# Kernel tuning notes

Hardware: AMD Instinct MI355X
Metric: run time of the kernel (lower is better)

Reference implementation:

```python
import jax, jax.numpy as jnp
import numpy as np

B, S, E, H = 2, 2048, 1024, 16
D = E // H  # head_dim = 64


def setup_inputs() -> dict:
    key = jax.random.key(0)
    ks = jax.random.split(key, 6)
    sc = 1.0 / np.sqrt(D)
    return {
        "x": jax.random.normal(ks[0], (B, S, E), dtype=jnp.float32),
        "Wq": jax.random.normal(ks[1], (D, D), dtype=jnp.float32) * sc,
        "Wk": jax.random.normal(ks[2], (D, D), dtype=jnp.float32) * sc,
        "Wv": jax.random.normal(ks[3], (D, D), dtype=jnp.float32) * sc,
        "Wo": jax.random.normal(ks[4], (E, E), dtype=jnp.float32) * (1.0 / np.sqrt(E)),
        "bo": jnp.zeros((E,), dtype=jnp.float32),
    }


def reference(x, Wq, Wk, Wv, Wo, bo):
    b, s, e = x.shape
    # split into heads: (B, H, S, D)
    xh = x.reshape(b, s, H, D).transpose(0, 2, 1, 3)
    # per-head linear projections (weights SHARED across heads); torch Linear: x @ W^T
    q = jnp.einsum('bhsd,ed->bhse', xh, Wq)
    k = jnp.einsum('bhsd,ed->bhse', xh, Wk)
    v = jnp.einsum('bhsd,ed->bhse', xh, Wv)
    # full attention matrix (B, H, S, S) — faithful to the naive original
    energy = jnp.einsum('bhqd,bhkd->bhqk', q, k)
    attn = jax.nn.softmax(energy / jnp.sqrt(jnp.asarray(D, x.dtype)), axis=-1)
    out = jnp.einsum('bhqk,bhkd->bhqd', attn, v)
    out = out.transpose(0, 2, 1, 3).reshape(b, s, e)
    return out @ Wo.T + bo
```

## Files before the change

### kernel.cpp

```cpp
#include <hip/hip_runtime.h>
#include <hip/hip_bf16.h>

#define B 2
#define S 2048
#define E 1024
#define H 16
#define D 64

typedef unsigned short ushort_t;
typedef __attribute__((ext_vector_type(8))) short bf16x8;
typedef __attribute__((ext_vector_type(4))) float f32x4;
typedef __attribute__((ext_vector_type(16))) float f32x16;

static __device__ __forceinline__ ushort_t f2bf(float f) {
    union { float f; unsigned u; } v; v.f = f;
    unsigned r = v.u + 0x7fffu + ((v.u >> 16) & 1u);
    return (ushort_t)(r >> 16);
}

#define MFMA(a, b, c)   __builtin_amdgcn_mfma_f32_16x16x32_bf16((a), (b), (c), 0, 0, 0)
#define MFMA32(a, b, c) __builtin_amdgcn_mfma_f32_32x32x16_bf16((a), (b), (c), 0, 0, 0)
#define PACKBF(hi, lo) __builtin_amdgcn_perm((hi), (lo), 0x07060302u)

__global__ __launch_bounds__(256) void cvt_w(
    const float* __restrict__ Wq, const float* __restrict__ Wk, const float* __restrict__ Wv,
    const float* __restrict__ Wo,
    ushort_t* __restrict__ wqb, ushort_t* __restrict__ wkb, ushort_t* __restrict__ wvb,
    ushort_t* __restrict__ wob)
{
    int gid = blockIdx.x, t = threadIdx.x;
    if (gid < 1024) {
        int i = gid * 1024 + t * 4;
        float4 f = *(const float4*)(Wo + i);
        ushort4 u; u.x = f2bf(f.x); u.y = f2bf(f.y); u.z = f2bf(f.z); u.w = f2bf(f.w);
        *(ushort4*)(wob + i) = u;
    } else {
        int idx = (gid - 1024) * 1024 + t * 4;
        int which = idx >> 12, off = idx & 4095;
        const float* src = (which == 0) ? Wq : (which == 1) ? Wk : Wv;
        ushort_t* dst    = (which == 0) ? wqb : (which == 1) ? wkb : wvb;
        float sc = (which == 0) ? 0.18033688011112042f : 1.0f;
        float4 f = *(const float4*)(src + off);
        ushort4 u; u.x = f2bf(f.x * sc); u.y = f2bf(f.y * sc);
        u.z = f2bf(f.z * sc); u.w = f2bf(f.w * sc);
        *(ushort4*)(dst + off) = u;
    }
}

__global__ __launch_bounds__(256) void qkv_proj(
    const float* __restrict__ x,
    const ushort_t* __restrict__ wq, const ushort_t* __restrict__ wk, const ushort_t* __restrict__ wv,
    ushort_t* __restrict__ q, ushort_t* __restrict__ k, ushort_t* __restrict__ vT)
{
    __shared__ ushort_t Xs[64][72];
    __shared__ ushort_t Wqs[64][72], Wks[64][72], Wvs[64][72];
    int t = threadIdx.x;
    int bh = blockIdx.y, b = bh >> 4, h = bh & 15;
    int s0 = blockIdx.x * 64;

    {
        int i = t >> 2, d0 = (t & 3) * 16;
        const float* xp = x + ((size_t)(b * S + s0 + i)) * E + h * D + d0;
        #pragma unroll
        for (int c = 0; c < 16; c += 4) {
            float4 f = *(const float4*)(xp + c);
            Xs[i][d0 + c + 0] = f2bf(f.x); Xs[i][d0 + c + 1] = f2bf(f.y);
            Xs[i][d0 + c + 2] = f2bf(f.z); Xs[i][d0 + c + 3] = f2bf(f.w);
        }
    }
    {
        int e = t >> 2, d0 = (t & 3) * 16;
        *(bf16x8*)&Wqs[e][d0]     = *(const bf16x8*)(wq + e * 64 + d0);
        *(bf16x8*)&Wqs[e][d0 + 8] = *(const bf16x8*)(wq + e * 64 + d0 + 8);
        *(bf16x8*)&Wks[e][d0]     = *(const bf16x8*)(wk + e * 64 + d0);
        *(bf16x8*)&Wks[e][d0 + 8] = *(const bf16x8*)(wk + e * 64 + d0 + 8);
        *(bf16x8*)&Wvs[e][d0]     = *(const bf16x8*)(wv + e * 64 + d0);
        *(bf16x8*)&Wvs[e][d0 + 8] = *(const bf16x8*)(wv + e * 64 + d0 + 8);
    }
    __syncthreads();

    int w = t >> 6, lane = t & 63, m = lane & 15, quad = lane >> 4;
    bf16x8 a0 = *(bf16x8*)&Xs[16 * w + m][quad * 8];
    bf16x8 a1 = *(bf16x8*)&Xs[16 * w + m][32 + quad * 8];
    f32x4 cq[4], ck[4], cv[4];
    #pragma unroll
    for (int nt = 0; nt < 4; nt++) { cq[nt] = (f32x4)0.f; ck[nt] = (f32x4)0.f; cv[nt] = (f32x4)0.f; }
    #pragma unroll
    for (int nt = 0; nt < 4; nt++) {
        bf16x8 b0, b1;
        b0 = *(bf16x8*)&Wqs[nt * 16 + m][quad * 8]; b1 = *(bf16x8*)&Wqs[nt * 16 + m][32 + quad * 8];
        cq[nt] = MFMA(a0, b0, cq[nt]); cq[nt] = MFMA(a1, b1, cq[nt]);
        b0 = *(bf16x8*)&Wks[nt * 16 + m][quad * 8]; b1 = *(bf16x8*)&Wks[nt * 16 + m][32 + quad * 8];
        ck[nt] = MFMA(a0, b0, ck[nt]); ck[nt] = MFMA(a1, b1, ck[nt]);
        b0 = *(bf16x8*)&Wvs[nt * 16 + m][quad * 8]; b1 = *(bf16x8*)&Wvs[nt * 16 + m][32 + quad * 8];
        cv[nt] = MFMA(a0, b0, cv[nt]); cv[nt] = MFMA(a1, b1, cv[nt]);
    }
    size_t base = (size_t)bh * S + s0;
    #pragma unroll
    for (int nt = 0; nt < 4; nt++)
        #pragma unroll
        for (int r = 0; r < 4; r++) {
            size_t idx = (base + 16 * w + quad * 4 + r) * D + nt * 16 + m;
            q[idx] = f2bf(cq[nt][r]);
            k[idx] = f2bf(ck[nt][r]);
        }
    __syncthreads();
    #pragma unroll
    for (int nt = 0; nt < 4; nt++)
        #pragma unroll
        for (int r = 0; r < 4; r++)
            Wvs[nt * 16 + m][16 * w + quad * 4 + r] = f2bf(cv[nt][r]);
    __syncthreads();
    {
        int d0 = t >> 2, sc = (t & 3) * 16;
        ushort_t* vp = vT + ((size_t)bh * D + d0) * S + s0 + sc;
        *(bf16x8*)(vp)     = *(bf16x8*)&Wvs[d0][sc];
        *(bf16x8*)(vp + 8) = *(bf16x8*)&Wvs[d0][sc + 8];
    }
}

__global__ __launch_bounds__(256) void flash_attn(
    const ushort_t* __restrict__ q, const ushort_t* __restrict__ k,
    const ushort_t* __restrict__ vT, ushort_t* __restrict__ ao)
{
    __shared__ ushort_t Ks[2][64][72];
    __shared__ ushort_t Vt[2][64][72];
    int t = threadIdx.x;
    int bh = blockIdx.y, b = bh >> 4, h = bh & 15;
    int q0 = blockIdx.x * 128;
    int w = t >> 6, lane = t & 63, l31 = lane & 31, half = lane >> 5;

    const ushort_t* qb = q + ((size_t)bh * S + q0) * D;
    const ushort_t* kb = k + (size_t)bh * S * D;
    const ushort_t* vb = vT + (size_t)bh * D * S;

    bf16x8 qf[4];
    {
        const ushort_t* qp = qb + (size_t)(w * 32 + l31) * D + half * 8;
        #pragma unroll
        for (int c = 0; c < 4; c++) qf[c] = *(const bf16x8*)(qp + c * 16);
    }

    f32x16 o0 = (f32x16)0.f, o1 = (f32x16)0.f;
    float lsum = 0.f;

    int sr = t >> 2, scc = (t & 3) * 16;
    bf16x8 kp0, kp1, vp0, vp1;

    {
        const ushort_t* kp = kb + (size_t)sr * D + scc;
        const ushort_t* vp = vb + (size_t)sr * S + scc;
        kp0 = *(const bf16x8*)(kp);     kp1 = *(const bf16x8*)(kp + 8);
        vp0 = *(const bf16x8*)(vp);     vp1 = *(const bf16x8*)(vp + 8);
        *(bf16x8*)&Ks[0][sr][scc]     = kp0;
        *(bf16x8*)&Ks[0][sr][scc + 8] = kp1;
        *(bf16x8*)&Vt[0][sr][scc]     = vp0;
        *(bf16x8*)&Vt[0][sr][scc + 8] = vp1;
    }
    __syncthreads();
    {
        const ushort_t* kp = kb + (size_t)(64 + sr) * D + scc;
        const ushort_t* vp = vb + (size_t)sr * S + 64 + scc;
        kp0 = *(const bf16x8*)(kp);     kp1 = *(const bf16x8*)(kp + 8);
        vp0 = *(const bf16x8*)(vp);     vp1 = *(const bf16x8*)(vp + 8);
    }

    const int NT = S / 64;
    for (int it = 0; it < NT; it++) {
        int p = it & 1;
        if (it + 1 < NT) {
            *(bf16x8*)&Ks[1 - p][sr][scc]     = kp0;
            *(bf16x8*)&Ks[1 - p][sr][scc + 8] = kp1;
            *(bf16x8*)&Vt[1 - p][sr][scc]     = vp0;
            *(bf16x8*)&Vt[1 - p][sr][scc + 8] = vp1;
        }
        if (it + 2 < NT) {
            int k0n = (it + 2) * 64;
            const ushort_t* kp = kb + (size_t)(k0n + sr) * D + scc;
            const ushort_t* vp = vb + (size_t)sr * S + k0n + scc;
            kp0 = *(const bf16x8*)(kp);     kp1 = *(const bf16x8*)(kp + 8);
            vp0 = *(const bf16x8*)(vp);     vp1 = *(const bf16x8*)(vp + 8);
        }

        union { unsigned u[4]; bf16x8 v; } pa[4];
        #pragma unroll
        for (int st = 0; st < 2; st++) {
            f32x16 e = (f32x16)0.f;
            #pragma unroll
            for (int c = 0; c < 4; c++) {
                bf16x8 ka = *(bf16x8*)&Ks[p][st * 32 + l31][c * 16 + half * 8];
                e = MFMA32(ka, qf[c], e);
            }
            unsigned pt[16];
            #pragma unroll
            for (int r = 0; r < 16; r++) {
                float pe = __builtin_amdgcn_exp2f(e[r]);
                unsigned msk = __float_as_uint(pe) & 0xffff0000u;
                lsum += __uint_as_float(msk);
                pt[r] = msk;
            }
            #pragma unroll
            for (int c2 = 0; c2 < 2; c2++) {
                int rb = c2 * 8;
                unsigned dA = PACKBF(pt[rb + 1], pt[rb + 0]);
                unsigned dB = PACKBF(pt[rb + 3], pt[rb + 2]);
                unsigned dC = PACKBF(pt[rb + 5], pt[rb + 4]);
                unsigned dD = PACKBF(pt[rb + 7], pt[rb + 6]);
                unsigned x1 = (unsigned)__shfl_xor((int)(half ? dA : dC), 32, 64);
                unsigned x2 = (unsigned)__shfl_xor((int)(half ? dB : dD), 32, 64);
                int kc = st * 2 + c2;
                pa[kc].u[0] = half ? x1 : dA;
                pa[kc].u[1] = half ? x2 : dB;
                pa[kc].u[2] = half ? dC : x1;
                pa[kc].u[3] = half ? dD : x2;
            }
        }

        #pragma unroll
        for (int kc = 0; kc < 4; kc++) {
            bf16x8 vf0 = *(bf16x8*)&Vt[p][l31][kc * 16 + half * 8];
            bf16x8 vf1 = *(bf16x8*)&Vt[p][32 + l31][kc * 16 + half * 8];
            o0 = MFMA32(pa[kc].v, vf0, o0);
            o1 = MFMA32(pa[kc].v, vf1, o1);
        }
        __syncthreads();
    }

    float lfull = lsum + __shfl_xor(lsum, 32, 64);
    float inv = 1.f / lfull;
    #pragma unroll
    for (int reg = 0; reg < 16; reg++) {
        int qrow = (reg & 3) + 8 * (reg >> 2) + 4 * half;
        float li = __shfl(inv, qrow, 64);
        int srow = q0 + w * 32 + qrow;
        size_t base = ((size_t)(b * S + srow)) * E + h * D + l31;
        ao[base]      = f2bf(o0[reg] * li);
        ao[base + 32] = f2bf(o1[reg] * li);
    }
}

__global__ __launch_bounds__(256) void out_proj(
    const ushort_t* __restrict__ A, const ushort_t* __restrict__ Wob,
    const float* __restrict__ bo, float* __restrict__ Y)
{
    __shared__ ushort_t As[128][72];
    __shared__ ushort_t Ws[64][72];
    int t = threadIdx.x;
    int n0 = blockIdx.x * 64, m0 = blockIdx.y * 128;
    int w = t >> 6, lane = t & 63, m = lane & 15, quad = lane >> 4;
    f32x4 acc[2][4];
    #pragma unroll
    for (int u = 0; u < 2; u++)
        #pragma unroll
        for (int nt = 0; nt < 4; nt++) acc[u][nt] = (f32x4)0.f;

    int ar = t >> 1, ac = (t & 1) * 32;
    int wr = t >> 2, wc = (t & 3) * 16;
    for (int k0 = 0; k0 < E; k0 += 64) {
        __syncthreads();
        {
            const ushort_t* ap = A + (size_t)(m0 + ar) * E + k0 + ac;
            #pragma unroll
            for (int i = 0; i < 4; i++)
                *(bf16x8*)&As[ar][ac + 8 * i] = *(const bf16x8*)(ap + 8 * i);
            const ushort_t* wp = Wob + (size_t)(n0 + wr) * E + k0 + wc;
            *(bf16x8*)&Ws[wr][wc]     = *(const bf16x8*)(wp);
            *(bf16x8*)&Ws[wr][wc + 8] = *(const bf16x8*)(wp + 8);
        }
        __syncthreads();
        #pragma unroll
        for (int h2 = 0; h2 < 2; h2++) {
            bf16x8 af[2];
            af[0] = *(bf16x8*)&As[w * 32 + m][h2 * 32 + quad * 8];
            af[1] = *(bf16x8*)&As[w * 32 + 16 + m][h2 * 32 + quad * 8];
            #pragma unroll
            for (int nt = 0; nt < 4; nt++) {
                bf16x8 bfr = *(bf16x8*)&Ws[nt * 16 + m][h2 * 32 + quad * 8];
                acc[0][nt] = MFMA(af[0], bfr, acc[0][nt]);
                acc[1][nt] = MFMA(af[1], bfr, acc[1][nt]);
            }
        }
    }
    #pragma unroll
    for (int u = 0; u < 2; u++)
        #pragma unroll
        for (int nt = 0; nt < 4; nt++)
            #pragma unroll
            for (int r = 0; r < 4; r++) {
                int row = m0 + w * 32 + u * 16 + quad * 4 + r;
                int col = n0 + nt * 16 + m;
                Y[(size_t)row * E + col] = acc[u][nt][r] + bo[col];
            }
}

extern "C" void kernel_launch(void* const* d_in, const int* in_sizes, int n_in,
                              void* d_out, int out_size, void* d_ws, size_t ws_size,
                              hipStream_t stream)
{
    const float* x  = (const float*)d_in[0];
    const float* Wq = (const float*)d_in[1];
    const float* Wk = (const float*)d_in[2];
    const float* Wv = (const float*)d_in[3];
    const float* Wo = (const float*)d_in[4];
    const float* bo = (const float*)d_in[5];
    float* Y = (float*)d_out;

    const size_t n = (size_t)B * H * S * D;
    ushort_t* qw  = (ushort_t*)d_ws;
    ushort_t* kw  = qw + n;
    ushort_t* vTw = kw + n;
    ushort_t* ao  = vTw + n;
    ushort_t* wob = ao + n;
    ushort_t* wqb = wob + (size_t)E * E;
    ushort_t* wkb = wqb + D * D;
    ushort_t* wvb = wkb + D * D;

    cvt_w<<<dim3(1024 + 12), 256, 0, stream>>>(Wq, Wk, Wv, Wo, wqb, wkb, wvb, wob);
    qkv_proj<<<dim3(S / 64, B * H), 256, 0, stream>>>(x, wqb, wkb, wvb, qw, kw, vTw);
    flash_attn<<<dim3(S / 128, B * H), 256, 0, stream>>>(qw, kw, vTw, ao);
    out_proj<<<dim3(E / 64, (B * S) / 128), 256, 0, stream>>>(ao, wob, bo, Y);
}
```

Before: 155.5 us.

## Load K fragments directly to registers and double-buffer out_proj LDS tiles

In flash_attn, each wave now loads its K MFMA fragments straight from global memory into registers, double-buffered via ping-pong arrays across iterations. This removes the K shared-memory staging and its LDS reads and writes, at the cost of more VGPRs and redundant global loads across the four waves. In out_proj, the A and W tiles are double-buffered in LDS with a register prefetch two steps ahead, leaving one barrier per k-step instead of two. This overlaps global loads with the MFMA work.

```diff
diff --git a/kernel.cpp b/kernel.cpp
--- a/kernel.cpp
+++ b/kernel.cpp
@@ -123,7 +123,6 @@
     const ushort_t* __restrict__ q, const ushort_t* __restrict__ k,
     const ushort_t* __restrict__ vT, ushort_t* __restrict__ ao)
 {
-    __shared__ ushort_t Ks[2][64][72];
     __shared__ ushort_t Vt[2][64][72];
     int t = threadIdx.x;
     int bh = blockIdx.y, b = bh >> 4, h = bh & 15;
@@ -145,41 +144,45 @@
     float lsum = 0.f;
 
     int sr = t >> 2, scc = (t & 3) * 16;
-    bf16x8 kp0, kp1, vp0, vp1;
-
-    {
-        const ushort_t* kp = kb + (size_t)sr * D + scc;
+    bf16x8 vp0, vp1;
+    const ushort_t* kfp = kb + (size_t)l31 * D + half * 8;
+
+    bf16x8 kfA[8], kfB[8];
+    #pragma unroll
+    for (int st = 0; st < 2; st++)
+        #pragma unroll
+        for (int c = 0; c < 4; c++)
+            kfA[st * 4 + c] = *(const bf16x8*)(kfp + (size_t)(st * 32) * D + c * 16);
+
+    {
         const ushort_t* vp = vb + (size_t)sr * S + scc;
-        kp0 = *(const bf16x8*)(kp);     kp1 = *(const bf16x8*)(kp + 8);
-        vp0 = *(const bf16x8*)(vp);     vp1 = *(const bf16x8*)(vp + 8);
-        *(bf16x8*)&Ks[0][sr][scc]     = kp0;
-        *(bf16x8*)&Ks[0][sr][scc + 8] = kp1;
+        vp0 = *(const bf16x8*)(vp);  vp1 = *(const bf16x8*)(vp + 8);
         *(bf16x8*)&Vt[0][sr][scc]     = vp0;
         *(bf16x8*)&Vt[0][sr][scc + 8] = vp1;
     }
     __syncthreads();
     {
-        const ushort_t* kp = kb + (size_t)(64 + sr) * D + scc;
         const ushort_t* vp = vb + (size_t)sr * S + 64 + scc;
-        kp0 = *(const bf16x8*)(kp);     kp1 = *(const bf16x8*)(kp + 8);
-        vp0 = *(const bf16x8*)(vp);     vp1 = *(const bf16x8*)(vp + 8);
+        vp0 = *(const bf16x8*)(vp);  vp1 = *(const bf16x8*)(vp + 8);
     }
 
     const int NT = S / 64;
-    for (int it = 0; it < NT; it++) {
-        int p = it & 1;
+    auto body = [&](bf16x8 (&kcur)[8], bf16x8 (&knxt)[8], int it, int p) {
         if (it + 1 < NT) {
-            *(bf16x8*)&Ks[1 - p][sr][scc]     = kp0;
-            *(bf16x8*)&Ks[1 - p][sr][scc + 8] = kp1;
             *(bf16x8*)&Vt[1 - p][sr][scc]     = vp0;
             *(bf16x8*)&Vt[1 - p][sr][scc + 8] = vp1;
         }
         if (it + 2 < NT) {
-            int k0n = (it + 2) * 64;
-            const ushort_t* kp = kb + (size_t)(k0n + sr) * D + scc;
-            const ushort_t* vp = vb + (size_t)sr * S + k0n + scc;
-            kp0 = *(const bf16x8*)(kp);     kp1 = *(const bf16x8*)(kp + 8);
-            vp0 = *(const bf16x8*)(vp);     vp1 = *(const bf16x8*)(vp + 8);
+            const ushort_t* vp = vb + (size_t)sr * S + (it + 2) * 64 + scc;
+            vp0 = *(const bf16x8*)(vp);  vp1 = *(const bf16x8*)(vp + 8);
+        }
+        if (it + 1 < NT) {
+            const ushort_t* kp = kfp + (size_t)(it + 1) * 64 * D;
+            #pragma unroll
+            for (int st = 0; st < 2; st++)
+                #pragma unroll
+                for (int c = 0; c < 4; c++)
+                    knxt[st * 4 + c] = *(const bf16x8*)(kp + (size_t)(st * 32) * D + c * 16);
         }
 
         union { unsigned u[4]; bf16x8 v; } pa[4];
@@ -187,10 +190,8 @@
         for (int st = 0; st < 2; st++) {
             f32x16 e = (f32x16)0.f;
             #pragma unroll
-            for (int c = 0; c < 4; c++) {
-                bf16x8 ka = *(bf16x8*)&Ks[p][st * 32 + l31][c * 16 + half * 8];
-                e = MFMA32(ka, qf[c], e);
-            }
+            for (int c = 0; c < 4; c++)
+                e = MFMA32(kcur[st * 4 + c], qf[c], e);
             unsigned pt[16];
             #pragma unroll
             for (int r = 0; r < 16; r++) {
@@ -224,6 +225,11 @@
             o1 = MFMA32(pa[kc].v, vf1, o1);
         }
         __syncthreads();
+    };
+
+    for (int it = 0; it < NT; it += 2) {
+        body(kfA, kfB, it, 0);
+        body(kfB, kfA, it + 1, 1);
     }
 
     float lfull = lsum + __shfl_xor(lsum, 32, 64);
@@ -243,8 +249,8 @@
     const ushort_t* __restrict__ A, const ushort_t* __restrict__ Wob,
     const float* __restrict__ bo, float* __restrict__ Y)
 {
-    __shared__ ushort_t As[128][72];
-    __shared__ ushort_t Ws[64][72];
+    __shared__ ushort_t As[2][128][72];
+    __shared__ ushort_t Ws[2][64][72];
     int t = threadIdx.x;
     int n0 = blockIdx.x * 64, m0 = blockIdx.y * 128;
     int w = t >> 6, lane = t & 63, m = lane & 15, quad = lane >> 4;
@@ -256,30 +262,53 @@
 
     int ar = t >> 1, ac = (t & 1) * 32;
     int wr = t >> 2, wc = (t & 3) * 16;
-    for (int k0 = 0; k0 < E; k0 += 64) {
-        __syncthreads();
-        {
-            const ushort_t* ap = A + (size_t)(m0 + ar) * E + k0 + ac;
-            #pragma unroll
-            for (int i = 0; i < 4; i++)
-                *(bf16x8*)&As[ar][ac + 8 * i] = *(const bf16x8*)(ap + 8 * i);
-            const ushort_t* wp = Wob + (size_t)(n0 + wr) * E + k0 + wc;
-            *(bf16x8*)&Ws[wr][wc]     = *(const bf16x8*)(wp);
-            *(bf16x8*)&Ws[wr][wc + 8] = *(const bf16x8*)(wp + 8);
-        }
-        __syncthreads();
+    const ushort_t* apb = A + (size_t)(m0 + ar) * E + ac;
+    const ushort_t* wpb = Wob + (size_t)(n0 + wr) * E + wc;
+
+    bf16x8 arg[4], wrg[2];
+    {
+        #pragma unroll
+        for (int i = 0; i < 4; i++) *(bf16x8*)&As[0][ar][ac + 8 * i] = *(const bf16x8*)(apb + 8 * i);
+        *(bf16x8*)&Ws[0][wr][wc]     = *(const bf16x8*)(wpb);
+        *(bf16x8*)&Ws[0][wr][wc + 8] = *(const bf16x8*)(wpb + 8);
+    }
+    __syncthreads();
+    {
+        #pragma unroll
+        for (int i = 0; i < 4; i++) arg[i] = *(const bf16x8*)(apb + 64 + 8 * i);
+        wrg[0] = *(const bf16x8*)(wpb + 64);
+        wrg[1] = *(const bf16x8*)(wpb + 64 + 8);
+    }
+
+    const int KT = E / 64;
+    for (int ks = 0; ks < KT; ks++) {
+        int p = ks & 1;
+        if (ks + 1 < KT) {
+            #pragma unroll
+            for (int i = 0; i < 4; i++) *(bf16x8*)&As[1 - p][ar][ac + 8 * i] = arg[i];
+            *(bf16x8*)&Ws[1 - p][wr][wc]     = wrg[0];
+            *(bf16x8*)&Ws[1 - p][wr][wc + 8] = wrg[1];
+        }
+        if (ks + 2 < KT) {
+            int off = (ks + 2) * 64;
+            #pragma unroll
+            for (int i = 0; i < 4; i++) arg[i] = *(const bf16x8*)(apb + off + 8 * i);
+            wrg[0] = *(const bf16x8*)(wpb + off);
+            wrg[1] = *(const bf16x8*)(wpb + off + 8);
+        }
         #pragma unroll
         for (int h2 = 0; h2 < 2; h2++) {
             bf16x8 af[2];
-            af[0] = *(bf16x8*)&As[w * 32 + m][h2 * 32 + quad * 8];
-            af[1] = *(bf16x8*)&As[w * 32 + 16 + m][h2 * 32 + quad * 8];
+            af[0] = *(bf16x8*)&As[p][w * 32 + m][h2 * 32 + quad * 8];
+            af[1] = *(bf16x8*)&As[p][w * 32 + 16 + m][h2 * 32 + quad * 8];
             #pragma unroll
             for (int nt = 0; nt < 4; nt++) {
-                bf16x8 bfr = *(bf16x8*)&Ws[nt * 16 + m][h2 * 32 + quad * 8];
+                bf16x8 bfr = *(bf16x8*)&Ws[p][nt * 16 + m][h2 * 32 + quad * 8];
                 acc[0][nt] = MFMA(af[0], bfr, acc[0][nt]);
                 acc[1][nt] = MFMA(af[1], bfr, acc[1][nt]);
             }
         }
+        __syncthreads();
     }
     #pragma unroll
     for (int u = 0; u < 2; u++)
```

After: 173.0 us. 11.3% more time.

## Double-buffer out_proj tiles with register prefetch and simplify softmax sum accumulation

Applied to the files above, without the earlier changes.

The output projection GEMM now uses two LDS buffers and prefetches the next K-tile into registers two steps ahead, so global loads overlap the MFMA work and one barrier per iteration is dropped. In attention, the row-sum masking of exp values to bf16 is removed, two partial sums are kept in parallel, and a constant fudge factor in the final reciprocal compensates for the truncation that PACKBF applies to the P values. This shortens the dependency chain in the softmax loop but changes numerics slightly and doubles LDS use in out_proj, which could lower occupancy.

```diff
diff --git a/kernel.cpp b/kernel.cpp
--- a/kernel.cpp
+++ b/kernel.cpp
@@ -142,7 +142,7 @@
     }
 
     f32x16 o0 = (f32x16)0.f, o1 = (f32x16)0.f;
-    float lsum = 0.f;
+    float2 ls2 = make_float2(0.f, 0.f);
 
     int sr = t >> 2, scc = (t & 3) * 16;
     bf16x8 kp0, kp1, vp0, vp1;
@@ -193,11 +193,12 @@
             }
             unsigned pt[16];
             #pragma unroll
-            for (int r = 0; r < 16; r++) {
-                float pe = __builtin_amdgcn_exp2f(e[r]);
-                unsigned msk = __float_as_uint(pe) & 0xffff0000u;
-                lsum += __uint_as_float(msk);
-                pt[r] = msk;
+            for (int r = 0; r < 16; r += 2) {
+                float pe0 = __builtin_amdgcn_exp2f(e[r]);
+                float pe1 = __builtin_amdgcn_exp2f(e[r + 1]);
+                ls2.x += pe0; ls2.y += pe1;
+                pt[r]     = __float_as_uint(pe0);
+                pt[r + 1] = __float_as_uint(pe1);
             }
             #pragma unroll
             for (int c2 = 0; c2 < 2; c2++) {
@@ -226,8 +227,9 @@
         __syncthreads();
     }
 
+    float lsum = ls2.x + ls2.y;
     float lfull = lsum + __shfl_xor(lsum, 32, 64);
-    float inv = 1.f / lfull;
+    float inv = 1.001953125f / lfull;
     #pragma unroll
     for (int reg = 0; reg < 16; reg++) {
         int qrow = (reg & 3) + 8 * (reg >> 2) + 4 * half;
@@ -243,8 +245,8 @@
     const ushort_t* __restrict__ A, const ushort_t* __restrict__ Wob,
     const float* __restrict__ bo, float* __restrict__ Y)
 {
-    __shared__ ushort_t As[128][72];
-    __shared__ ushort_t Ws[64][72];
+    __shared__ ushort_t As[2][128][72];
+    __shared__ ushort_t Ws[2][64][72];
     int t = threadIdx.x;
     int n0 = blockIdx.x * 64, m0 = blockIdx.y * 128;
     int w = t >> 6, lane = t & 63, m = lane & 15, quad = lane >> 4;
@@ -256,30 +258,53 @@
 
     int ar = t >> 1, ac = (t & 1) * 32;
     int wr = t >> 2, wc = (t & 3) * 16;
-    for (int k0 = 0; k0 < E; k0 += 64) {
-        __syncthreads();
-        {
-            const ushort_t* ap = A + (size_t)(m0 + ar) * E + k0 + ac;
-            #pragma unroll
-            for (int i = 0; i < 4; i++)
-                *(bf16x8*)&As[ar][ac + 8 * i] = *(const bf16x8*)(ap + 8 * i);
-            const ushort_t* wp = Wob + (size_t)(n0 + wr) * E + k0 + wc;
-            *(bf16x8*)&Ws[wr][wc]     = *(const bf16x8*)(wp);
-            *(bf16x8*)&Ws[wr][wc + 8] = *(const bf16x8*)(wp + 8);
-        }
-        __syncthreads();
+    const ushort_t* apb = A + (size_t)(m0 + ar) * E + ac;
+    const ushort_t* wpb = Wob + (size_t)(n0 + wr) * E + wc;
+
+    bf16x8 arg[4], wrg[2];
+    {
+        #pragma unroll
+        for (int i = 0; i < 4; i++) *(bf16x8*)&As[0][ar][ac + 8 * i] = *(const bf16x8*)(apb + 8 * i);
+        *(bf16x8*)&Ws[0][wr][wc]     = *(const bf16x8*)(wpb);
+        *(bf16x8*)&Ws[0][wr][wc + 8] = *(const bf16x8*)(wpb + 8);
+    }
+    __syncthreads();
+    {
+        #pragma unroll
+        for (int i = 0; i < 4; i++) arg[i] = *(const bf16x8*)(apb + 64 + 8 * i);
+        wrg[0] = *(const bf16x8*)(wpb + 64);
+        wrg[1] = *(const bf16x8*)(wpb + 64 + 8);
+    }
+
+    const int KT = E / 64;
+    for (int ks = 0; ks < KT; ks++) {
+        int p = ks & 1;
+        if (ks + 1 < KT) {
+            #pragma unroll
+            for (int i = 0; i < 4; i++) *(bf16x8*)&As[1 - p][ar][ac + 8 * i] = arg[i];
+            *(bf16x8*)&Ws[1 - p][wr][wc]     = wrg[0];
+            *(bf16x8*)&Ws[1 - p][wr][wc + 8] = wrg[1];
+        }
+        if (ks + 2 < KT) {
+            int off = (ks + 2) * 64;
+            #pragma unroll
+            for (int i = 0; i < 4; i++) arg[i] = *(const bf16x8*)(apb + off + 8 * i);
+            wrg[0] = *(const bf16x8*)(wpb + off);
+            wrg[1] = *(const bf16x8*)(wpb + off + 8);
+        }
         #pragma unroll
         for (int h2 = 0; h2 < 2; h2++) {
             bf16x8 af[2];
-            af[0] = *(bf16x8*)&As[w * 32 + m][h2 * 32 + quad * 8];
-            af[1] = *(bf16x8*)&As[w * 32 + 16 + m][h2 * 32 + quad * 8];
+            af[0] = *(bf16x8*)&As[p][w * 32 + m][h2 * 32 + quad * 8];
+            af[1] = *(bf16x8*)&As[p][w * 32 + 16 + m][h2 * 32 + quad * 8];
             #pragma unroll
             for (int nt = 0; nt < 4; nt++) {
-                bf16x8 bfr = *(bf16x8*)&Ws[nt * 16 + m][h2 * 32 + quad * 8];
+                bf16x8 bfr = *(bf16x8*)&Ws[p][nt * 16 + m][h2 * 32 + quad * 8];
                 acc[0][nt] = MFMA(af[0], bfr, acc[0][nt]);
                 acc[1][nt] = MFMA(af[1], bfr, acc[1][nt]);
             }
         }
+        __syncthreads();
     }
     #pragma unroll
     for (int u = 0; u < 2; u++)
```

New measurement: 152.2 us. 2.1% less time.
